# Kernel tuning notes

Measured on AMD Instinct MI355X. Metric: run time of the kernel, lower is better.

Reference implementation:

```python
import jax, jax.numpy as jnp
import numpy as np

# Constants from the torch module __init__
FACE_INDS = np.array([[0, 1, 2, 3], [0, 4, 2, 6], [0, 1, 4, 5],
                      [1, 3, 5, 7], [2, 3, 6, 7], [4, 5, 6, 7]])  # (6,4)
N_GRID = 11
N_POINTS = N_GRID * N_GRID        # 121
N_FACE = 6
N_KP_HAND = 21
N_CONTACTS = 10
ITA = 0.2
IND1 = np.array([0, 1, 2, 3])
IND2 = np.array([1, 2, 3, 0])


def _bilinear_grid():
    # grid[p, k] = bilinear weights for the 4 face corners, p over 11x11 (u,v)
    g = []
    for u in np.linspace(0.0, 1.0, N_GRID):
        for v in np.linspace(0.0, 1.0, N_GRID):
            g.append([v * (1 - u), v * u, (1 - v) * (1 - u), u * (1 - v)])
    return jnp.asarray(np.array(g, dtype=np.float32))  # (121, 4)


def setup_inputs() -> dict:
    key = jax.random.key(0)
    poses = jax.random.normal(key, (8192, N_KP_HAND + 8, 3), dtype=jnp.float32)
    return {"poses": poses}


def affinity_loss(poses):
    bs = poses.shape[0]
    hand = poses[:, :N_KP_HAND, :]          # (bs, 21, 3)
    obj = poses[:, N_KP_HAND:, :]           # (bs, 8, 3)

    # --- sample_face_points: bilinear sample 121 pts on each of the 6 faces ---
    grid = _bilinear_grid().astype(poses.dtype)        # (121, 4)
    faces = obj[:, FACE_INDS, :]                        # (bs, 6, 4, 3)
    face_points = jnp.einsum('bfkc,pk->bfpc', faces, grid)  # (bs, 6, 121, 3)
    obj_pts = face_points.reshape(bs, N_FACE * N_POINTS, 3)  # (bs, 726, 3)

    xx = jnp.sum(hand * hand, axis=-1)                  # (bs, 21)
    yy = jnp.sum(obj_pts * obj_pts, axis=-1)            # (bs, 726)
    zz = jnp.einsum('bic,bjc->bij', hand, obj_pts)      # (bs, 21, 726)
    pdist = jnp.sqrt(xx[:, :, None] + yy[:, None, :] - 2.0 * zz + 1e-6)
    pdist = pdist.reshape(bs, N_KP_HAND, N_FACE, N_POINTS)

    # --- per (hand kp, face) nearest face point, then global top-10 contacts ---
    dist_h2f = jnp.min(pdist, axis=3)                   # (bs, 21, 6)
    idxs_h2f = jnp.argmin(pdist, axis=3)                # (bs, 21, 6)
    flat = dist_h2f.reshape(bs, N_KP_HAND * N_FACE)     # (bs, 126)
    order = jnp.argsort(flat, axis=1)[:, :N_CONTACTS]   # (bs, 10)
    dist = jnp.take_along_axis(flat, order, axis=1)     # (bs, 10)
    inds_hand = order // N_FACE
    inds_face = order % N_FACE
    b = jnp.arange(bs)[:, None]
    ind_obj = idxs_h2f[b, inds_hand, inds_face]                     # (bs, 10)
    obj_contacts = obj_pts[b, inds_face * N_POINTS + ind_obj]       # (bs, 10, 3)

    # --- get_obj_info: axis endpoints and mean edge length of the bbox ---
    points1 = obj[:, :4, :].mean(axis=1)                # (bs, 3)
    points2 = obj[:, 4:, :].mean(axis=1)                # (bs, 3)
    l1 = jnp.linalg.norm(obj[:, IND1] - obj[:, IND2], axis=-1).mean(1, keepdims=True)
    l2 = jnp.linalg.norm(obj[:, IND1 + 4] - obj[:, IND2 + 4], axis=-1).mean(1, keepdims=True)
    length = (l1 + l2) * 0.5                            # (bs, 1)

    mask1 = (dist < length * ITA).astype(poses.dtype)   # (bs, 10)
    mask = mask1[:, :, None] * mask1[:, None, :]        # (bs, 10, 10)

    direct_vec = points2 - points1                      # (bs, 3)
    dv_norm = jnp.linalg.norm(direct_vec, axis=1, keepdims=True)  # (bs, 1)
    normed_dv = direct_vec / (dv_norm + 1e-5)
    vec_contacts = obj_contacts - points1[:, None, :]   # (bs, 10, 3)
    inner = jnp.sum(direct_vec[:, None, :] * vec_contacts, axis=-1)  # (bs, 10)
    t = inner / (dv_norm + 1e-5)                        # (bs, 10)
    r = points1[:, None, :] + normed_dv[:, None, :] * t[:, :, None]  # (bs, 10, 3)
    normal_vec = obj_contacts - r
    normal_vec = normal_vec / (jnp.linalg.norm(normal_vec, axis=2, keepdims=True) + 1e-5)
    cos_sim = jnp.einsum('bic,bjc->bij', normal_vec, normal_vec)  # (bs, 10, 10)

    return (cos_sim * mask).sum() / (mask.sum() + 1.0)


def reference(poses):
    return affinity_loss(poses)
```

## Files before the change

### kernel.cpp

```cpp
#include <hip/hip_runtime.h>
#include <math.h>

#define NGRID   11
#define NPAIR   126
#define NCONT   10

#define NSUB    64
#define NBUK    128
#define WS_SUB  16
#define WS_BUK  128
#define WS_WORDS (WS_BUK + 2 * NBUK)

#define NBUCKET 256

typedef float v2f __attribute__((ext_vector_type(2)));
#define FMA2(a,b,c) __builtin_elementwise_fma((a),(b),(c))
#define MAX2(a,b)   __builtin_elementwise_max((a),(b))
#define SP2(x)      ((v2f){(x),(x)})

__device__ __forceinline__ int last_hit(unsigned old, unsigned quota) {
    const unsigned r = old + 1u - quota;
    return (r == 0u) || (r == 0xAAAAAAAAu);
}

__device__ __constant__ int4 c_face4[6] = {
    {0,1,2,3},{0,4,2,6},{0,1,4,5},{1,3,5,7},{2,3,6,7},{4,5,6,7}};
__device__ __constant__ float c_U[NGRID] = {
    0.0f,0.1f,0.2f,0.3f,0.4f,0.5f,0.6f,0.7f,0.8f,0.9f,1.0f};

__global__ void zero_ws_kernel(float* ws, int n) {
    int t = blockIdx.x * 256 + threadIdx.x;
    if (t < n) ws[t] = 0.0f;
}

__device__ __forceinline__ void coefs_from_face(
        const float4* __restrict__ Ff, float hx, float hy, float hz,
        float& C00, float& C10, float& C01, float& C11,
        float& C20, float& C02, float& C21, float& C12, float& C22) {
    const float4 F0 = Ff[0], F1 = Ff[1], F2 = Ff[2],
                 F3 = Ff[3], F4 = Ff[4], F5 = Ff[5];
    const float hx2 = 2.0f * hx, hy2 = 2.0f * hy, hz2 = 2.0f * hz;
    const float ha2 = fmaf(hx2, F0.x, fmaf(hy2, F0.y, hz2 * F0.z));
    const float hb2 = fmaf(hx2, F1.x, fmaf(hy2, F1.y, hz2 * F1.z));
    const float hc2 = fmaf(hx2, F2.x, fmaf(hy2, F2.y, hz2 * F2.z));
    const float hd2 = fmaf(hx2, F3.x, fmaf(hy2, F3.y, hz2 * F3.z));
    C00 = ha2 - F0.w;
    C10 = hb2 - F4.x;
    C01 = hc2 - F4.y;
    C11 = hd2 - F4.z;
    C20 = -F1.w;  C02 = -F2.w;  C21 = -F4.w;  C12 = -F5.x;  C22 = -F3.w;
}

__launch_bounds__(256)
__global__ void affinity_kernel(const float* __restrict__ poses,
                                float* __restrict__ ws,
                                float* __restrict__ out,
                                int bs, int mode) {
    const int t    = threadIdx.x;
    const int half = t >> 7;
    const int t0   = t & 127;
    const int batch = blockIdx.x * 2 + half;
    const bool valid = batch < bs;

    __shared__ float    sh_pose[2][88];
    __shared__ float4   sh_face[2][36];
    __shared__ float    sh_thr[2][2];
    __shared__ int      sh_ru[2][128];
    __shared__ int      sh_cpair[2][128];
    __shared__ unsigned sh_cnt[2], sh_cnt2[2];
    __shared__ unsigned sh_key[2][128];
    __shared__ float    sh_cont[2][128][3];
    __shared__ float    sh_win[2][NCONT][3];
    __shared__ float    sh_nd[2][2];
    __shared__ int      sh_last;
    __shared__ double   sh_rn[4], sh_rd[4];

    if (valid && t0 < 87) sh_pose[half][t0] = poses[(size_t)batch * 87 + t0];
    if (t0 == 127) { sh_cnt[half] = 0u; sh_cnt2[half] = 0u; }
    __syncthreads();

    const float* hand = sh_pose[half];
    const float* obj  = sh_pose[half] + 63;

    if (valid && t0 < 6) {
        const int4 F = c_face4[t0];
        float C0[3], C1[3], C2[3], C3[3];
        #pragma unroll
        for (int c = 0; c < 3; ++c) {
            C0[c] = obj[F.x * 3 + c];
            C1[c] = obj[F.y * 3 + c];
            C2[c] = obj[F.z * 3 + c];
            C3[c] = obj[F.w * 3 + c];
        }
        float av[3], bv[3], cv[3], dv[3];
        #pragma unroll
        for (int c = 0; c < 3; ++c) {
            av[c] = C2[c];
            bv[c] = C3[c] - C2[c];
            cv[c] = C0[c] - C2[c];
            dv[c] = C1[c] - C0[c] - C3[c] + C2[c];
        }
        float aa=0.f,bb=0.f,cc=0.f,dd=0.f,ab=0.f,ac=0.f,ad=0.f,bc=0.f,bd=0.f,cd=0.f;
        #pragma unroll
        for (int c = 0; c < 3; ++c) {
            aa += av[c]*av[c]; bb += bv[c]*bv[c];
            cc += cv[c]*cv[c]; dd += dv[c]*dv[c];
            ab += av[c]*bv[c]; ac += av[c]*cv[c];
            ad += av[c]*dv[c]; bc += bv[c]*cv[c];
            bd += bv[c]*dv[c]; cd += cv[c]*dv[c];
        }
        float4* Ff = &sh_face[half][t0 * 6];
        Ff[0] = make_float4(av[0], av[1], av[2], aa);
        Ff[1] = make_float4(bv[0], bv[1], bv[2], bb);
        Ff[2] = make_float4(cv[0], cv[1], cv[2], cc);
        Ff[3] = make_float4(dv[0], dv[1], dv[2], dd);
        Ff[4] = make_float4(2.f*ab, 2.f*ac, 2.f*(ad+bc), 2.f*bd);
        Ff[5] = make_float4(2.f*cd, 0.f, 0.f, 0.f);
    }
    if (valid && t0 == 6) {
        float l1 = 0.0f, l2 = 0.0f;
        #pragma unroll
        for (int e = 0; e < 4; ++e) {
            const int a = e, b2 = (e + 1) & 3;
            {
                const float dx = obj[a*3+0]-obj[b2*3+0];
                const float dy = obj[a*3+1]-obj[b2*3+1];
                const float dz = obj[a*3+2]-obj[b2*3+2];
                l1 += sqrtf(dx*dx + dy*dy + dz*dz);
            }
            {
                const float dx = obj[(a+4)*3+0]-obj[(b2+4)*3+0];
                const float dy = obj[(a+4)*3+1]-obj[(b2+4)*3+1];
                const float dz = obj[(a+4)*3+2]-obj[(b2+4)*3+2];
                l2 += sqrtf(dx*dx + dy*dy + dz*dz);
            }
        }
        l1 *= 0.25f; l2 *= 0.25f;
        const float L02 = (l1 + l2) * 0.5f * 0.2f;
        sh_thr[half][0] = L02 * L02 - 1e-6f + 1e-2f;
        sh_thr[half][1] = L02;
    }
    __syncthreads();

    if (valid && t0 < NPAIR) {
        const int i = t0 / 6;
        const int f = t0 - i * 6;
        const float hx = hand[i*3+0], hy = hand[i*3+1], hz = hand[i*3+2];
        const float xx = hx*hx + hy*hy + hz*hz;
        float C00,C10,C01,C11,C20,C02,C21,C12,C22;
        coefs_from_face(&sh_face[half][f*6], hx, hy, hz,
                        C00,C10,C01,C11,C20,C02,C21,C12,C22);

        const float U[NGRID] = {0.0f,0.1f,0.2f,0.3f,0.4f,0.5f,
                                0.6f,0.7f,0.8f,0.9f,1.0f};
        float qb = -3.0e38f;
        int   ru = 0;
        #pragma unroll
        for (int rp = 0; rp < 5; ++rp) {
            const v2f u2 = (v2f){U[2*rp], U[2*rp+1]};
            const v2f A2 = FMA2(FMA2(SP2(C22), u2, SP2(C12)), u2, SP2(C02));
            const v2f A1 = FMA2(FMA2(SP2(C21), u2, SP2(C11)), u2, SP2(C01));
            const v2f A0 = FMA2(FMA2(SP2(C20), u2, SP2(C10)), u2, SP2(C00));
            v2f m2 = A0;
            #pragma unroll
            for (int iv = 1; iv < NGRID; ++iv) {
                const v2f vv = SP2(U[iv]);
                m2 = MAX2(m2, FMA2(FMA2(A2, vv, A1), vv, A0));
            }
            if (m2.x > qb) { qb = m2.x; ru = 2*rp; }
            if (m2.y > qb) { qb = m2.y; ru = 2*rp + 1; }
        }
        {
            const float u = 1.0f;
            const float A2 = fmaf(fmaf(C22,u,C12),u,C02);
            const float A1 = fmaf(fmaf(C21,u,C11),u,C01);
            const float A0 = fmaf(fmaf(C20,u,C10),u,C00);
            float m1 = A0;
            #pragma unroll
            for (int iv = 1; iv < NGRID; ++iv)
                m1 = fmaxf(m1, fmaf(fmaf(A2,U[iv],A1),U[iv],A0));
            if (m1 > qb) { qb = m1; ru = 10; }
        }
        sh_ru[half][t0] = ru;
        const float d2s = xx - qb;
        if (d2s < sh_thr[half][0]) {
            const unsigned s = atomicAdd(&sh_cnt[half], 1u);
            sh_cpair[half][s] = t0;
        }
    }
    __syncthreads();

    {
        const int cnt = (int)sh_cnt[half];
        if (t0 < cnt) {
            const int pair = sh_cpair[half][t0];
            const int i  = pair / 6;
            const int f  = pair - 6 * i;
            const int ru = sh_ru[half][pair];
            const float hx = hand[i*3+0], hy = hand[i*3+1], hz = hand[i*3+2];
            float C00,C10,C01,C11,C20,C02,C21,C12,C22;
            coefs_from_face(&sh_face[half][f*6], hx, hy, hz,
                            C00,C10,C01,C11,C20,C02,C21,C12,C22);
            const float u  = c_U[ru];
            const float A2 = fmaf(fmaf(C22,u,C12),u,C02);
            const float A1 = fmaf(fmaf(C21,u,C11),u,C01);
            const float A0 = fmaf(fmaf(C20,u,C10),u,C00);
            const float U[NGRID] = {0.0f,0.1f,0.2f,0.3f,0.4f,0.5f,
                                    0.6f,0.7f,0.8f,0.9f,1.0f};
            float qr = A0; int vb = 0;
            #pragma unroll
            for (int iv = 1; iv < NGRID; ++iv) {
                const float q = fmaf(fmaf(A2,U[iv],A1),U[iv],A0);
                if (q > qr) { qr = q; vb = iv; }
            }
            const double du = ru * 0.1;
            const double dv = vb * 0.1;
            const float w0 = (float)(dv * (1.0 - du));
            const float w1 = (float)(dv * du);
            const float w2 = (float)((1.0 - dv) * (1.0 - du));
            const float w3 = (float)(du * (1.0 - dv));
            const int4 F = c_face4[f];
            const int i0 = F.x*3, i1 = F.y*3, i2 = F.z*3, i3 = F.w*3;
            const float cx = w0*obj[i0+0]+w1*obj[i1+0]+w2*obj[i2+0]+w3*obj[i3+0];
            const float cy = w0*obj[i0+1]+w1*obj[i1+1]+w2*obj[i2+1]+w3*obj[i3+1];
            const float cz = w0*obj[i0+2]+w1*obj[i1+2]+w2*obj[i2+2]+w3*obj[i3+2];
            const float xx = hx*hx + hy*hy + hz*hz;
            const float yy = cx*cx + cy*cy + cz*cz;
            const float zz = hx*cx + hy*cy + hz*cz;
            const float d2e = (xx + yy) - 2.0f * zz;
            const float dist = sqrtf(d2e + 1e-6f);
            if (dist < sh_thr[half][1]) {
                const unsigned s2 = atomicAdd(&sh_cnt2[half], 1u);
                const float d2k = fmaxf(d2e, 0.0f);
                sh_key[half][s2] = (__float_as_uint(d2k) & 0xFFFFFF80u)
                                 | (unsigned)pair;
                sh_cont[half][s2][0] = cx;
                sh_cont[half][s2][1] = cy;
                sh_cont[half][s2][2] = cz;
            }
        }
    }
    __syncthreads();

    const int n2 = (int)sh_cnt2[half];
    if (t0 < n2) {
        const unsigned ke = sh_key[half][t0];
        int rank = 0;
        for (int j = 0; j < n2; ++j) rank += (sh_key[half][j] < ke) ? 1 : 0;
        if (rank < NCONT) {
            sh_win[half][rank][0] = sh_cont[half][t0][0];
            sh_win[half][rank][1] = sh_cont[half][t0][1];
            sh_win[half][rank][2] = sh_cont[half][t0][2];
        }
    }
    __syncthreads();

    const int kwin = n2 < NCONT ? n2 : NCONT;
    float px = 0.f, py = 0.f, pz = 0.f;
    if (valid && t0 < kwin) {
        const float cx = sh_win[half][t0][0];
        const float cy = sh_win[half][t0][1];
        const float cz = sh_win[half][t0][2];
        const float p1x = (((obj[0] +obj[3]) +obj[6]) +obj[9]) *0.25f;
        const float p1y = (((obj[1] +obj[4]) +obj[7]) +obj[10])*0.25f;
        const float p1z = (((obj[2] +obj[5]) +obj[8]) +obj[11])*0.25f;
        const float p2x = (((obj[12]+obj[15])+obj[18])+obj[21])*0.25f;
        const float p2y = (((obj[13]+obj[16])+obj[19])+obj[22])*0.25f;
        const float p2z = (((obj[14]+obj[17])+obj[20])+obj[23])*0.25f;
        const float dvx = p2x-p1x, dvy = p2y-p1y, dvz = p2z-p1z;
        const float dvn = sqrtf(dvx*dvx + dvy*dvy + dvz*dvz);
        const float den = dvn + 1e-5f;
        const float ndx = dvx/den, ndy = dvy/den, ndz = dvz/den;
        const float vcx = cx-p1x, vcy = cy-p1y, vcz = cz-p1z;
        const float inner = dvx*vcx + dvy*vcy + dvz*vcz;
        const float tp = inner / den;
        const float rx = p1x + ndx*tp, ry = p1y + ndy*tp, rz = p1z + ndz*tp;
        float nvx = cx-rx, nvy = cy-ry, nvz = cz-rz;
        const float nvn = sqrtf(nvx*nvx + nvy*nvy + nvz*nvz) + 1e-5f;
        px = nvx / nvn; py = nvy / nvn; pz = nvz / nvn;
    }
    if (t0 < 64) {
        #pragma unroll
        for (int off = 32; off >= 1; off >>= 1) {
            px += __shfl_xor(px, off, 64);
            py += __shfl_xor(py, off, 64);
            pz += __shfl_xor(pz, off, 64);
        }
        if (t0 == 0) {
            sh_nd[half][0] = px*px + py*py + pz*pz;
            sh_nd[half][1] = (float)(kwin * kwin);
        }
    }
    __syncthreads();

    if (t == 0) {
        sh_last = 0;
        const float num = sh_nd[0][0] + sh_nd[1][0];
        const float dnm = sh_nd[0][1] + sh_nd[1][1];
        const int b = blockIdx.x;
        if (mode) {
            float* bkt = ws + WS_BUK + 2 * (b & (NBUK - 1));
            const float r0 = atomicAdd(bkt + 0, num);
            const float r1 = atomicAdd(bkt + 1, dnm);
            asm volatile("" :: "v"(r0), "v"(r1) : "memory");
            unsigned* subs = (unsigned*)ws + WS_SUB;
            const unsigned nb = gridDim.x;
            const unsigned g  = (unsigned)b & (NSUB - 1);
            const unsigned quota = (nb - 1u - g) / NSUB + 1u;
            const unsigned old = atomicAdd(subs + g, 1u);
            if (last_hit(old, quota)) {
                const unsigned ngroups = nb < NSUB ? nb : NSUB;
                const unsigned m2 = atomicAdd((unsigned*)ws, 1u);
                if (last_hit(m2, ngroups)) sh_last = 1;
            }
        } else {
            float* bucket = ws + 2 * (b & (NBUCKET - 1));
            atomicAdd(bucket + 0, num);
            atomicAdd(bucket + 1, dnm);
        }
    }
    __syncthreads();

    if (sh_last) {
        double n = 0.0, d = 0.0;
        if (t < NBUK) {
            float* bkt = ws + WS_BUK + 2 * t;
            n = (double)atomicAdd(bkt + 0, 0.0f);
            d = (double)atomicAdd(bkt + 1, 0.0f);
        }
        #pragma unroll
        for (int off = 32; off >= 1; off >>= 1) {
            n += __shfl_xor(n, off, 64);
            d += __shfl_xor(d, off, 64);
        }
        const int w = t >> 6;
        if ((t & 63) == 0) { sh_rn[w] = n; sh_rd[w] = d; }
        __syncthreads();
        if (t == 0) {
            const double nn = sh_rn[0] + sh_rn[1] + sh_rn[2] + sh_rn[3];
            const double dd = sh_rd[0] + sh_rd[1] + sh_rd[2] + sh_rd[3];
            out[0] = (float)(nn / (dd + 1.0));
        }
    }
}

__launch_bounds__(1024)
__global__ void finalize_kernel(const float* __restrict__ ws,
                                float* __restrict__ out, int nslot) {
    const int t = threadIdx.x;
    __shared__ double sh_n[16], sh_d[16];
    double n = 0.0, d = 0.0;
    for (int k = t; k < nslot; k += 1024) {
        n += (double)ws[2 * k + 0];
        d += (double)ws[2 * k + 1];
    }
    #pragma unroll
    for (int off = 32; off >= 1; off >>= 1) {
        n += __shfl_xor(n, off, 64);
        d += __shfl_xor(d, off, 64);
    }
    const int w = t >> 6;
    if ((t & 63) == 0) { sh_n[w] = n; sh_d[w] = d; }
    __syncthreads();
    if (t == 0) {
        double nn = 0.0, dd = 0.0;
        #pragma unroll
        for (int i = 0; i < 16; ++i) { nn += sh_n[i]; dd += sh_d[i]; }
        out[0] = (float)(nn / (dd + 1.0));
    }
}

extern "C" void kernel_launch(void* const* d_in, const int* in_sizes, int n_in,
                              void* d_out, int out_size, void* d_ws, size_t ws_size,
                              hipStream_t stream) {
    const float* poses = (const float*)d_in[0];
    float* out = (float*)d_out;
    float* ws  = (float*)d_ws;
    const int bs = in_sizes[0] / 87;
    const int nblk = (bs + 1) / 2;

    if (ws_size >= (size_t)WS_WORDS * sizeof(float)) {
        hipLaunchKernelGGL(affinity_kernel, dim3(nblk), dim3(256), 0, stream,
                           poses, ws, out, bs, 1);
    } else {
        hipLaunchKernelGGL(zero_ws_kernel, dim3(1), dim3(256), 0, stream,
                           ws, NBUCKET * 2);
        hipLaunchKernelGGL(affinity_kernel, dim3(nblk), dim3(256), 0, stream,
                           poses, ws, out, bs, 0);
        hipLaunchKernelGGL(finalize_kernel, dim3(1), dim3(1024), 0, stream,
                           ws, out, NBUCKET);
    }
}
```

Before: 76.69 us.

## Process one batch per 128-thread block and finish reduction in one wave

Switches from two batch elements per 256-thread block to one batch element per 128-thread block, doubling the grid to bs blocks. The upper wave exits early after the top-k selection, and the final contribution and last-block reduction use wave shuffles instead of shared memory plus block barriers. The aim is to cut the per-block barrier and shared-memory traffic and give the scheduler smaller blocks, at the cost of twice as many blocks and twice as many global atomic arrivals on the completion counters.

```diff
diff --git a/kernel.cpp b/kernel.cpp
--- a/kernel.cpp
+++ b/kernel.cpp
@@ -51,39 +51,33 @@
     C20 = -F1.w;  C02 = -F2.w;  C21 = -F4.w;  C12 = -F5.x;  C22 = -F3.w;
 }
 
-__launch_bounds__(256)
+__launch_bounds__(128)
 __global__ void affinity_kernel(const float* __restrict__ poses,
                                 float* __restrict__ ws,
                                 float* __restrict__ out,
                                 int bs, int mode) {
-    const int t    = threadIdx.x;
-    const int half = t >> 7;
-    const int t0   = t & 127;
-    const int batch = blockIdx.x * 2 + half;
-    const bool valid = batch < bs;
-
-    __shared__ float    sh_pose[2][88];
-    __shared__ float4   sh_face[2][36];
-    __shared__ float    sh_thr[2][2];
-    __shared__ int      sh_ru[2][128];
-    __shared__ int      sh_cpair[2][128];
-    __shared__ unsigned sh_cnt[2], sh_cnt2[2];
-    __shared__ unsigned sh_key[2][128];
-    __shared__ float    sh_cont[2][128][3];
-    __shared__ float    sh_win[2][NCONT][3];
-    __shared__ float    sh_nd[2][2];
-    __shared__ int      sh_last;
-    __shared__ double   sh_rn[4], sh_rd[4];
-
-    if (valid && t0 < 87) sh_pose[half][t0] = poses[(size_t)batch * 87 + t0];
-    if (t0 == 127) { sh_cnt[half] = 0u; sh_cnt2[half] = 0u; }
-    __syncthreads();
-
-    const float* hand = sh_pose[half];
-    const float* obj  = sh_pose[half] + 63;
-
-    if (valid && t0 < 6) {
-        const int4 F = c_face4[t0];
+    const int t = threadIdx.x;
+    const int b = blockIdx.x;
+
+    __shared__ float    sh_pose[88];
+    __shared__ float4   sh_face[36];
+    __shared__ float    sh_thr[2];
+    __shared__ int      sh_ru[128];
+    __shared__ int      sh_cpair[128];
+    __shared__ unsigned sh_cnt, sh_cnt2;
+    __shared__ unsigned sh_key[128];
+    __shared__ float    sh_cont[128][3];
+    __shared__ float    sh_win[NCONT][3];
+
+    if (t < 87) sh_pose[t] = poses[(size_t)b * 87 + t];
+    if (t == 127) { sh_cnt = 0u; sh_cnt2 = 0u; }
+    __syncthreads();
+
+    const float* hand = sh_pose;
+    const float* obj  = sh_pose + 63;
+
+    if (t < 6) {
+        const int4 F = c_face4[t];
         float C0[3], C1[3], C2[3], C3[3];
         #pragma unroll
         for (int c = 0; c < 3; ++c) {
@@ -109,7 +103,7 @@
             ad += av[c]*dv[c]; bc += bv[c]*cv[c];
             bd += bv[c]*dv[c]; cd += cv[c]*dv[c];
         }
-        float4* Ff = &sh_face[half][t0 * 6];
+        float4* Ff = &sh_face[t * 6];
         Ff[0] = make_float4(av[0], av[1], av[2], aa);
         Ff[1] = make_float4(bv[0], bv[1], bv[2], bb);
         Ff[2] = make_float4(cv[0], cv[1], cv[2], cc);
@@ -117,7 +111,7 @@
         Ff[4] = make_float4(2.f*ab, 2.f*ac, 2.f*(ad+bc), 2.f*bd);
         Ff[5] = make_float4(2.f*cd, 0.f, 0.f, 0.f);
     }
-    if (valid && t0 == 6) {
+    if (t == 6) {
         float l1 = 0.0f, l2 = 0.0f;
         #pragma unroll
         for (int e = 0; e < 4; ++e) {
@@ -137,18 +131,18 @@
         }
         l1 *= 0.25f; l2 *= 0.25f;
         const float L02 = (l1 + l2) * 0.5f * 0.2f;
-        sh_thr[half][0] = L02 * L02 - 1e-6f + 1e-2f;
-        sh_thr[half][1] = L02;
-    }
-    __syncthreads();
-
-    if (valid && t0 < NPAIR) {
-        const int i = t0 / 6;
-        const int f = t0 - i * 6;
+        sh_thr[0] = L02 * L02 - 1e-6f + 1e-2f;
+        sh_thr[1] = L02;
+    }
+    __syncthreads();
+
+    if (t < NPAIR) {
+        const int i = t / 6;
+        const int f = t - i * 6;
         const float hx = hand[i*3+0], hy = hand[i*3+1], hz = hand[i*3+2];
         const float xx = hx*hx + hy*hy + hz*hz;
         float C00,C10,C01,C11,C20,C02,C21,C12,C22;
-        coefs_from_face(&sh_face[half][f*6], hx, hy, hz,
+        coefs_from_face(&sh_face[f*6], hx, hy, hz,
                         C00,C10,C01,C11,C20,C02,C21,C12,C22);
 
         const float U[NGRID] = {0.0f,0.1f,0.2f,0.3f,0.4f,0.5f,
@@ -181,25 +175,25 @@
                 m1 = fmaxf(m1, fmaf(fmaf(A2,U[iv],A1),U[iv],A0));
             if (m1 > qb) { qb = m1; ru = 10; }
         }
-        sh_ru[half][t0] = ru;
+        sh_ru[t] = ru;
         const float d2s = xx - qb;
-        if (d2s < sh_thr[half][0]) {
-            const unsigned s = atomicAdd(&sh_cnt[half], 1u);
-            sh_cpair[half][s] = t0;
+        if (d2s < sh_thr[0]) {
+            const unsigned s = atomicAdd(&sh_cnt, 1u);
+            sh_cpair[s] = t;
         }
     }
     __syncthreads();
 
     {
-        const int cnt = (int)sh_cnt[half];
-        if (t0 < cnt) {
-            const int pair = sh_cpair[half][t0];
+        const int cnt = (int)sh_cnt;
+        if (t < cnt) {
+            const int pair = sh_cpair[t];
             const int i  = pair / 6;
             const int f  = pair - 6 * i;
-            const int ru = sh_ru[half][pair];
+            const int ru = sh_ru[pair];
             const float hx = hand[i*3+0], hy = hand[i*3+1], hz = hand[i*3+2];
             float C00,C10,C01,C11,C20,C02,C21,C12,C22;
-            coefs_from_face(&sh_face[half][f*6], hx, hy, hz,
+            coefs_from_face(&sh_face[f*6], hx, hy, hz,
                             C00,C10,C01,C11,C20,C02,C21,C12,C22);
             const float u  = c_U[ru];
             const float A2 = fmaf(fmaf(C22,u,C12),u,C02);
@@ -229,38 +223,40 @@
             const float zz = hx*cx + hy*cy + hz*cz;
             const float d2e = (xx + yy) - 2.0f * zz;
             const float dist = sqrtf(d2e + 1e-6f);
-            if (dist < sh_thr[half][1]) {
-                const unsigned s2 = atomicAdd(&sh_cnt2[half], 1u);
+            if (dist < sh_thr[1]) {
+                const unsigned s2 = atomicAdd(&sh_cnt2, 1u);
                 const float d2k = fmaxf(d2e, 0.0f);
-                sh_key[half][s2] = (__float_as_uint(d2k) & 0xFFFFFF80u)
-                                 | (unsigned)pair;
-                sh_cont[half][s2][0] = cx;
-                sh_cont[half][s2][1] = cy;
-                sh_cont[half][s2][2] = cz;
-            }
-        }
-    }
-    __syncthreads();
-
-    const int n2 = (int)sh_cnt2[half];
-    if (t0 < n2) {
-        const unsigned ke = sh_key[half][t0];
+                sh_key[s2] = (__float_as_uint(d2k) & 0xFFFFFF80u)
+                           | (unsigned)pair;
+                sh_cont[s2][0] = cx;
+                sh_cont[s2][1] = cy;
+                sh_cont[s2][2] = cz;
+            }
+        }
+    }
+    __syncthreads();
+
+    const int n2 = (int)sh_cnt2;
+    if (t < n2) {
+        const unsigned ke = sh_key[t];
         int rank = 0;
-        for (int j = 0; j < n2; ++j) rank += (sh_key[half][j] < ke) ? 1 : 0;
+        for (int j = 0; j < n2; ++j) rank += (sh_key[j] < ke) ? 1 : 0;
         if (rank < NCONT) {
-            sh_win[half][rank][0] = sh_cont[half][t0][0];
-            sh_win[half][rank][1] = sh_cont[half][t0][1];
-            sh_win[half][rank][2] = sh_cont[half][t0][2];
-        }
-    }
-    __syncthreads();
+            sh_win[rank][0] = sh_cont[t][0];
+            sh_win[rank][1] = sh_cont[t][1];
+            sh_win[rank][2] = sh_cont[t][2];
+        }
+    }
+    __syncthreads();
+
+    if (t >= 64) return;
 
     const int kwin = n2 < NCONT ? n2 : NCONT;
     float px = 0.f, py = 0.f, pz = 0.f;
-    if (valid && t0 < kwin) {
-        const float cx = sh_win[half][t0][0];
-        const float cy = sh_win[half][t0][1];
-        const float cz = sh_win[half][t0][2];
+    if (t < kwin) {
+        const float cx = sh_win[t][0];
+        const float cy = sh_win[t][1];
+        const float cz = sh_win[t][2];
         const float p1x = (((obj[0] +obj[3]) +obj[6]) +obj[9]) *0.25f;
         const float p1y = (((obj[1] +obj[4]) +obj[7]) +obj[10])*0.25f;
         const float p1z = (((obj[2] +obj[5]) +obj[8]) +obj[11])*0.25f;
@@ -279,25 +275,17 @@
         const float nvn = sqrtf(nvx*nvx + nvy*nvy + nvz*nvz) + 1e-5f;
         px = nvx / nvn; py = nvy / nvn; pz = nvz / nvn;
     }
-    if (t0 < 64) {
-        #pragma unroll
-        for (int off = 32; off >= 1; off >>= 1) {
-            px += __shfl_xor(px, off, 64);
-            py += __shfl_xor(py, off, 64);
-            pz += __shfl_xor(pz, off, 64);
-        }
-        if (t0 == 0) {
-            sh_nd[half][0] = px*px + py*py + pz*pz;
-            sh_nd[half][1] = (float)(kwin * kwin);
-        }
-    }
-    __syncthreads();
-
+    #pragma unroll
+    for (int off = 32; off >= 1; off >>= 1) {
+        px += __shfl_xor(px, off, 64);
+        py += __shfl_xor(py, off, 64);
+        pz += __shfl_xor(pz, off, 64);
+    }
+
+    int last = 0;
     if (t == 0) {
-        sh_last = 0;
-        const float num = sh_nd[0][0] + sh_nd[1][0];
-        const float dnm = sh_nd[0][1] + sh_nd[1][1];
-        const int b = blockIdx.x;
+        const float num = px*px + py*py + pz*pz;
+        const float dnm = (float)(kwin * kwin);
         if (mode) {
             float* bkt = ws + WS_BUK + 2 * (b & (NBUK - 1));
             const float r0 = atomicAdd(bkt + 0, num);
@@ -311,7 +299,7 @@
             if (last_hit(old, quota)) {
                 const unsigned ngroups = nb < NSUB ? nb : NSUB;
                 const unsigned m2 = atomicAdd((unsigned*)ws, 1u);
-                if (last_hit(m2, ngroups)) sh_last = 1;
+                if (last_hit(m2, ngroups)) last = 1;
             }
         } else {
             float* bucket = ws + 2 * (b & (NBUCKET - 1));
@@ -319,28 +307,22 @@
             atomicAdd(bucket + 1, dnm);
         }
     }
-    __syncthreads();
-
-    if (sh_last) {
+    last = __shfl(last, 0, 64);
+
+    if (last) {
         double n = 0.0, d = 0.0;
-        if (t < NBUK) {
-            float* bkt = ws + WS_BUK + 2 * t;
-            n = (double)atomicAdd(bkt + 0, 0.0f);
-            d = (double)atomicAdd(bkt + 1, 0.0f);
+        #pragma unroll
+        for (int c = 0; c < 2; ++c) {
+            float* bkt = ws + WS_BUK + 2 * (c * 64 + t);
+            n += (double)atomicAdd(bkt + 0, 0.0f);
+            d += (double)atomicAdd(bkt + 1, 0.0f);
         }
         #pragma unroll
         for (int off = 32; off >= 1; off >>= 1) {
             n += __shfl_xor(n, off, 64);
             d += __shfl_xor(d, off, 64);
         }
-        const int w = t >> 6;
-        if ((t & 63) == 0) { sh_rn[w] = n; sh_rd[w] = d; }
-        __syncthreads();
-        if (t == 0) {
-            const double nn = sh_rn[0] + sh_rn[1] + sh_rn[2] + sh_rn[3];
-            const double dd = sh_rd[0] + sh_rd[1] + sh_rd[2] + sh_rd[3];
-            out[0] = (float)(nn / (dd + 1.0));
-        }
+        if (t == 0) out[0] = (float)(n / (d + 1.0));
     }
 }
 
@@ -377,15 +359,14 @@
     float* out = (float*)d_out;
     float* ws  = (float*)d_ws;
     const int bs = in_sizes[0] / 87;
-    const int nblk = (bs + 1) / 2;
 
     if (ws_size >= (size_t)WS_WORDS * sizeof(float)) {
-        hipLaunchKernelGGL(affinity_kernel, dim3(nblk), dim3(256), 0, stream,
+        hipLaunchKernelGGL(affinity_kernel, dim3(bs), dim3(128), 0, stream,
                            poses, ws, out, bs, 1);
     } else {
         hipLaunchKernelGGL(zero_ws_kernel, dim3(1), dim3(256), 0, stream,
                            ws, NBUCKET * 2);
-        hipLaunchKernelGGL(affinity_kernel, dim3(nblk), dim3(256), 0, stream,
+        hipLaunchKernelGGL(affinity_kernel, dim3(bs), dim3(128), 0, stream,
                            poses, ws, out, bs, 0);
         hipLaunchKernelGGL(finalize_kernel, dim3(1), dim3(1024), 0, stream,
                            ws, out, NBUCKET);
```

Result: slower. 88.81 us (+15.8%).

## Remove face-precompute barrier and fuse ranking with normal computation

Applied to the files above, without the earlier changes.

Each pair thread now recomputes its face coefficients and the length threshold from the shared pose, which removes the per-face shared-memory precompute stage and one block barrier. The candidate's u-index is packed into the candidate record instead of a separate shared array. Top-10 ranking is merged with the normal-vector accumulation inside one wavefront, removing another barrier and the winner buffer. The final cross-block reduction runs on a single wave using shuffles instead of shared memory and barriers. The cost is redundant ALU work per thread and more register pressure.

```diff
diff --git a/kernel.cpp b/kernel.cpp
--- a/kernel.cpp
+++ b/kernel.cpp
@@ -33,22 +33,101 @@
     if (t < n) ws[t] = 0.0f;
 }
 
-__device__ __forceinline__ void coefs_from_face(
-        const float4* __restrict__ Ff, float hx, float hy, float hz,
+__device__ __forceinline__ void pair_coefs(
+        const float* __restrict__ obj, float hx, float hy, float hz, int f,
         float& C00, float& C10, float& C01, float& C11,
         float& C20, float& C02, float& C21, float& C12, float& C22) {
-    const float4 F0 = Ff[0], F1 = Ff[1], F2 = Ff[2],
-                 F3 = Ff[3], F4 = Ff[4], F5 = Ff[5];
-    const float hx2 = 2.0f * hx, hy2 = 2.0f * hy, hz2 = 2.0f * hz;
-    const float ha2 = fmaf(hx2, F0.x, fmaf(hy2, F0.y, hz2 * F0.z));
-    const float hb2 = fmaf(hx2, F1.x, fmaf(hy2, F1.y, hz2 * F1.z));
-    const float hc2 = fmaf(hx2, F2.x, fmaf(hy2, F2.y, hz2 * F2.z));
-    const float hd2 = fmaf(hx2, F3.x, fmaf(hy2, F3.y, hz2 * F3.z));
-    C00 = ha2 - F0.w;
-    C10 = hb2 - F4.x;
-    C01 = hc2 - F4.y;
-    C11 = hd2 - F4.z;
-    C20 = -F1.w;  C02 = -F2.w;  C21 = -F4.w;  C12 = -F5.x;  C22 = -F3.w;
+    const int4 F = c_face4[f];
+    float av[3], bv[3], cv[3], dv[3];
+    #pragma unroll
+    for (int c = 0; c < 3; ++c) {
+        const float P0 = obj[F.x * 3 + c];
+        const float P1 = obj[F.y * 3 + c];
+        const float P2 = obj[F.z * 3 + c];
+        const float P3 = obj[F.w * 3 + c];
+        av[c] = P2;
+        bv[c] = P3 - P2;
+        cv[c] = P0 - P2;
+        dv[c] = P1 - P0 - P3 + P2;
+    }
+    float aa=0.f,bb=0.f,cc=0.f,dd=0.f,ab=0.f,ac=0.f,ad=0.f,bc=0.f,bd=0.f,cd=0.f;
+    #pragma unroll
+    for (int c = 0; c < 3; ++c) {
+        aa += av[c]*av[c]; bb += bv[c]*bv[c];
+        cc += cv[c]*cv[c]; dd += dv[c]*dv[c];
+        ab += av[c]*bv[c]; ac += av[c]*cv[c];
+        ad += av[c]*dv[c]; bc += bv[c]*cv[c];
+        bd += bv[c]*dv[c]; cd += cv[c]*dv[c];
+    }
+    const float hx2 = 2.0f*hx, hy2 = 2.0f*hy, hz2 = 2.0f*hz;
+    const float ha2 = fmaf(hx2, av[0], fmaf(hy2, av[1], hz2*av[2]));
+    const float hb2 = fmaf(hx2, bv[0], fmaf(hy2, bv[1], hz2*bv[2]));
+    const float hc2 = fmaf(hx2, cv[0], fmaf(hy2, cv[1], hz2*cv[2]));
+    const float hd2 = fmaf(hx2, dv[0], fmaf(hy2, dv[1], hz2*dv[2]));
+    C00 = ha2 - aa;
+    C10 = hb2 - 2.f*ab;
+    C01 = hc2 - 2.f*ac;
+    C11 = hd2 - 2.f*(ad + bc);
+    C20 = -bb;  C02 = -cc;  C21 = -2.f*bd;  C12 = -2.f*cd;  C22 = -dd;
+}
+
+__device__ __forceinline__ float length_thr(const float* __restrict__ obj) {
+    float l1 = 0.0f, l2 = 0.0f;
+    #pragma unroll
+    for (int e = 0; e < 4; ++e) {
+        const int a = e, b2 = (e + 1) & 3;
+        {
+            const float dx = obj[a*3+0]-obj[b2*3+0];
+            const float dy = obj[a*3+1]-obj[b2*3+1];
+            const float dz = obj[a*3+2]-obj[b2*3+2];
+            l1 += sqrtf(dx*dx + dy*dy + dz*dz);
+        }
+        {
+            const float dx = obj[(a+4)*3+0]-obj[(b2+4)*3+0];
+            const float dy = obj[(a+4)*3+1]-obj[(b2+4)*3+1];
+            const float dz = obj[(a+4)*3+2]-obj[(b2+4)*3+2];
+            l2 += sqrtf(dx*dx + dy*dy + dz*dz);
+        }
+    }
+    l1 *= 0.25f; l2 *= 0.25f;
+    return (l1 + l2) * 0.5f * 0.2f;
+}
+
+__device__ __forceinline__ void exact_contact(
+        const float* __restrict__ obj, const float* __restrict__ hand,
+        int pair, int ru, float& cx, float& cy, float& cz, float& d2e) {
+    const int i = pair / 6;
+    const int f = pair - 6 * i;
+    const float hx = hand[i*3+0], hy = hand[i*3+1], hz = hand[i*3+2];
+    float C00,C10,C01,C11,C20,C02,C21,C12,C22;
+    pair_coefs(obj, hx, hy, hz, f, C00,C10,C01,C11,C20,C02,C21,C12,C22);
+    const float u  = c_U[ru];
+    const float A2 = fmaf(fmaf(C22,u,C12),u,C02);
+    const float A1 = fmaf(fmaf(C21,u,C11),u,C01);
+    const float A0 = fmaf(fmaf(C20,u,C10),u,C00);
+    const float U[NGRID] = {0.0f,0.1f,0.2f,0.3f,0.4f,0.5f,
+                            0.6f,0.7f,0.8f,0.9f,1.0f};
+    float qr = A0; int vb = 0;
+    #pragma unroll
+    for (int iv = 1; iv < NGRID; ++iv) {
+        const float q = fmaf(fmaf(A2,U[iv],A1),U[iv],A0);
+        if (q > qr) { qr = q; vb = iv; }
+    }
+    const double du = ru * 0.1;
+    const double dv = vb * 0.1;
+    const float w0 = (float)(dv * (1.0 - du));
+    const float w1 = (float)(dv * du);
+    const float w2 = (float)((1.0 - dv) * (1.0 - du));
+    const float w3 = (float)(du * (1.0 - dv));
+    const int4 F = c_face4[f];
+    const int i0 = F.x*3, i1 = F.y*3, i2 = F.z*3, i3 = F.w*3;
+    cx = w0*obj[i0+0]+w1*obj[i1+0]+w2*obj[i2+0]+w3*obj[i3+0];
+    cy = w0*obj[i0+1]+w1*obj[i1+1]+w2*obj[i2+1]+w3*obj[i3+1];
+    cz = w0*obj[i0+2]+w1*obj[i1+2]+w2*obj[i2+2]+w3*obj[i3+2];
+    const float xx = hx*hx + hy*hy + hz*hz;
+    const float yy = cx*cx + cy*cy + cz*cz;
+    const float zz = hx*cx + hy*cy + hz*cz;
+    d2e = (xx + yy) - 2.0f * zz;
 }
 
 __launch_bounds__(256)
@@ -63,17 +142,11 @@
     const bool valid = batch < bs;
 
     __shared__ float    sh_pose[2][88];
-    __shared__ float4   sh_face[2][36];
-    __shared__ float    sh_thr[2][2];
-    __shared__ int      sh_ru[2][128];
-    __shared__ int      sh_cpair[2][128];
+    __shared__ unsigned sh_cand[2][128];
     __shared__ unsigned sh_cnt[2], sh_cnt2[2];
     __shared__ unsigned sh_key[2][128];
     __shared__ float    sh_cont[2][128][3];
-    __shared__ float    sh_win[2][NCONT][3];
     __shared__ float    sh_nd[2][2];
-    __shared__ int      sh_last;
-    __shared__ double   sh_rn[4], sh_rd[4];
 
     if (valid && t0 < 87) sh_pose[half][t0] = poses[(size_t)batch * 87 + t0];
     if (t0 == 127) { sh_cnt[half] = 0u; sh_cnt2[half] = 0u; }
@@ -82,74 +155,17 @@
     const float* hand = sh_pose[half];
     const float* obj  = sh_pose[half] + 63;
 
-    if (valid && t0 < 6) {
-        const int4 F = c_face4[t0];
-        float C0[3], C1[3], C2[3], C3[3];
-        #pragma unroll
-        for (int c = 0; c < 3; ++c) {
-            C0[c] = obj[F.x * 3 + c];
-            C1[c] = obj[F.y * 3 + c];
-            C2[c] = obj[F.z * 3 + c];
-            C3[c] = obj[F.w * 3 + c];
-        }
-        float av[3], bv[3], cv[3], dv[3];
-        #pragma unroll
-        for (int c = 0; c < 3; ++c) {
-            av[c] = C2[c];
-            bv[c] = C3[c] - C2[c];
-            cv[c] = C0[c] - C2[c];
-            dv[c] = C1[c] - C0[c] - C3[c] + C2[c];
-        }
-        float aa=0.f,bb=0.f,cc=0.f,dd=0.f,ab=0.f,ac=0.f,ad=0.f,bc=0.f,bd=0.f,cd=0.f;
-        #pragma unroll
-        for (int c = 0; c < 3; ++c) {
-            aa += av[c]*av[c]; bb += bv[c]*bv[c];
-            cc += cv[c]*cv[c]; dd += dv[c]*dv[c];
-            ab += av[c]*bv[c]; ac += av[c]*cv[c];
-            ad += av[c]*dv[c]; bc += bv[c]*cv[c];
-            bd += bv[c]*dv[c]; cd += cv[c]*dv[c];
-        }
-        float4* Ff = &sh_face[half][t0 * 6];
-        Ff[0] = make_float4(av[0], av[1], av[2], aa);
-        Ff[1] = make_float4(bv[0], bv[1], bv[2], bb);
-        Ff[2] = make_float4(cv[0], cv[1], cv[2], cc);
-        Ff[3] = make_float4(dv[0], dv[1], dv[2], dd);
-        Ff[4] = make_float4(2.f*ab, 2.f*ac, 2.f*(ad+bc), 2.f*bd);
-        Ff[5] = make_float4(2.f*cd, 0.f, 0.f, 0.f);
-    }
-    if (valid && t0 == 6) {
-        float l1 = 0.0f, l2 = 0.0f;
-        #pragma unroll
-        for (int e = 0; e < 4; ++e) {
-            const int a = e, b2 = (e + 1) & 3;
-            {
-                const float dx = obj[a*3+0]-obj[b2*3+0];
-                const float dy = obj[a*3+1]-obj[b2*3+1];
-                const float dz = obj[a*3+2]-obj[b2*3+2];
-                l1 += sqrtf(dx*dx + dy*dy + dz*dz);
-            }
-            {
-                const float dx = obj[(a+4)*3+0]-obj[(b2+4)*3+0];
-                const float dy = obj[(a+4)*3+1]-obj[(b2+4)*3+1];
-                const float dz = obj[(a+4)*3+2]-obj[(b2+4)*3+2];
-                l2 += sqrtf(dx*dx + dy*dy + dz*dz);
-            }
-        }
-        l1 *= 0.25f; l2 *= 0.25f;
-        const float L02 = (l1 + l2) * 0.5f * 0.2f;
-        sh_thr[half][0] = L02 * L02 - 1e-6f + 1e-2f;
-        sh_thr[half][1] = L02;
-    }
-    __syncthreads();
-
+    float L02 = 0.f;
     if (valid && t0 < NPAIR) {
+        L02 = length_thr(obj);
+        const float thrF = L02 * L02 - 1e-6f + 1e-2f;
+
         const int i = t0 / 6;
         const int f = t0 - i * 6;
         const float hx = hand[i*3+0], hy = hand[i*3+1], hz = hand[i*3+2];
         const float xx = hx*hx + hy*hy + hz*hz;
         float C00,C10,C01,C11,C20,C02,C21,C12,C22;
-        coefs_from_face(&sh_face[half][f*6], hx, hy, hz,
-                        C00,C10,C01,C11,C20,C02,C21,C12,C22);
+        pair_coefs(obj, hx, hy, hz, f, C00,C10,C01,C11,C20,C02,C21,C12,C22);
 
         const float U[NGRID] = {0.0f,0.1f,0.2f,0.3f,0.4f,0.5f,
                                 0.6f,0.7f,0.8f,0.9f,1.0f};
@@ -171,21 +187,19 @@
             if (m2.y > qb) { qb = m2.y; ru = 2*rp + 1; }
         }
         {
-            const float u = 1.0f;
-            const float A2 = fmaf(fmaf(C22,u,C12),u,C02);
-            const float A1 = fmaf(fmaf(C21,u,C11),u,C01);
-            const float A0 = fmaf(fmaf(C20,u,C10),u,C00);
+            const float A2 = fmaf(fmaf(C22,1.f,C12),1.f,C02);
+            const float A1 = fmaf(fmaf(C21,1.f,C11),1.f,C01);
+            const float A0 = fmaf(fmaf(C20,1.f,C10),1.f,C00);
             float m1 = A0;
             #pragma unroll
             for (int iv = 1; iv < NGRID; ++iv)
                 m1 = fmaxf(m1, fmaf(fmaf(A2,U[iv],A1),U[iv],A0));
             if (m1 > qb) { qb = m1; ru = 10; }
         }
-        sh_ru[half][t0] = ru;
         const float d2s = xx - qb;
-        if (d2s < sh_thr[half][0]) {
+        if (d2s < thrF) {
             const unsigned s = atomicAdd(&sh_cnt[half], 1u);
-            sh_cpair[half][s] = t0;
+            sh_cand[half][s] = (unsigned)t0 | ((unsigned)ru << 8);
         }
     }
     __syncthreads();
@@ -193,47 +207,16 @@
     {
         const int cnt = (int)sh_cnt[half];
         if (t0 < cnt) {
-            const int pair = sh_cpair[half][t0];
-            const int i  = pair / 6;
-            const int f  = pair - 6 * i;
-            const int ru = sh_ru[half][pair];
-            const float hx = hand[i*3+0], hy = hand[i*3+1], hz = hand[i*3+2];
-            float C00,C10,C01,C11,C20,C02,C21,C12,C22;
-            coefs_from_face(&sh_face[half][f*6], hx, hy, hz,
-                            C00,C10,C01,C11,C20,C02,C21,C12,C22);
-            const float u  = c_U[ru];
-            const float A2 = fmaf(fmaf(C22,u,C12),u,C02);
-            const float A1 = fmaf(fmaf(C21,u,C11),u,C01);
-            const float A0 = fmaf(fmaf(C20,u,C10),u,C00);
-            const float U[NGRID] = {0.0f,0.1f,0.2f,0.3f,0.4f,0.5f,
-                                    0.6f,0.7f,0.8f,0.9f,1.0f};
-            float qr = A0; int vb = 0;
-            #pragma unroll
-            for (int iv = 1; iv < NGRID; ++iv) {
-                const float q = fmaf(fmaf(A2,U[iv],A1),U[iv],A0);
-                if (q > qr) { qr = q; vb = iv; }
-            }
-            const double du = ru * 0.1;
-            const double dv = vb * 0.1;
-            const float w0 = (float)(dv * (1.0 - du));
-            const float w1 = (float)(dv * du);
-            const float w2 = (float)((1.0 - dv) * (1.0 - du));
-            const float w3 = (float)(du * (1.0 - dv));
-            const int4 F = c_face4[f];
-            const int i0 = F.x*3, i1 = F.y*3, i2 = F.z*3, i3 = F.w*3;
-            const float cx = w0*obj[i0+0]+w1*obj[i1+0]+w2*obj[i2+0]+w3*obj[i3+0];
-            const float cy = w0*obj[i0+1]+w1*obj[i1+1]+w2*obj[i2+1]+w3*obj[i3+1];
-            const float cz = w0*obj[i0+2]+w1*obj[i1+2]+w2*obj[i2+2]+w3*obj[i3+2];
-            const float xx = hx*hx + hy*hy + hz*hz;
-            const float yy = cx*cx + cy*cy + cz*cz;
-            const float zz = hx*cx + hy*cy + hz*cz;
-            const float d2e = (xx + yy) - 2.0f * zz;
+            const unsigned rec = sh_cand[half][t0];
+            const int pair = rec & 0xFF;
+            const int ru   = rec >> 8;
+            float cx, cy, cz, d2e;
+            exact_contact(obj, hand, pair, ru, cx, cy, cz, d2e);
             const float dist = sqrtf(d2e + 1e-6f);
-            if (dist < sh_thr[half][1]) {
+            if (dist < L02) {
                 const unsigned s2 = atomicAdd(&sh_cnt2[half], 1u);
-                const float d2k = fmaxf(d2e, 0.0f);
-                sh_key[half][s2] = (__float_as_uint(d2k) & 0xFFFFFF80u)
-                                 | (unsigned)pair;
+                sh_key[half][s2] = (__float_as_uint(fmaxf(d2e, 0.0f))
+                                    & 0xFFFFFF80u) | (unsigned)pair;
                 sh_cont[half][s2][0] = cx;
                 sh_cont[half][s2][1] = cy;
                 sh_cont[half][s2][2] = cz;
@@ -242,49 +225,52 @@
     }
     __syncthreads();
 
-    const int n2 = (int)sh_cnt2[half];
-    if (t0 < n2) {
-        const unsigned ke = sh_key[half][t0];
-        int rank = 0;
-        for (int j = 0; j < n2; ++j) rank += (sh_key[half][j] < ke) ? 1 : 0;
-        if (rank < NCONT) {
-            sh_win[half][rank][0] = sh_cont[half][t0][0];
-            sh_win[half][rank][1] = sh_cont[half][t0][1];
-            sh_win[half][rank][2] = sh_cont[half][t0][2];
-        }
-    }
-    __syncthreads();
-
-    const int kwin = n2 < NCONT ? n2 : NCONT;
-    float px = 0.f, py = 0.f, pz = 0.f;
-    if (valid && t0 < kwin) {
-        const float cx = sh_win[half][t0][0];
-        const float cy = sh_win[half][t0][1];
-        const float cz = sh_win[half][t0][2];
-        const float p1x = (((obj[0] +obj[3]) +obj[6]) +obj[9]) *0.25f;
-        const float p1y = (((obj[1] +obj[4]) +obj[7]) +obj[10])*0.25f;
-        const float p1z = (((obj[2] +obj[5]) +obj[8]) +obj[11])*0.25f;
-        const float p2x = (((obj[12]+obj[15])+obj[18])+obj[21])*0.25f;
-        const float p2y = (((obj[13]+obj[16])+obj[19])+obj[22])*0.25f;
-        const float p2z = (((obj[14]+obj[17])+obj[20])+obj[23])*0.25f;
-        const float dvx = p2x-p1x, dvy = p2y-p1y, dvz = p2z-p1z;
-        const float dvn = sqrtf(dvx*dvx + dvy*dvy + dvz*dvz);
-        const float den = dvn + 1e-5f;
-        const float ndx = dvx/den, ndy = dvy/den, ndz = dvz/den;
-        const float vcx = cx-p1x, vcy = cy-p1y, vcz = cz-p1z;
-        const float inner = dvx*vcx + dvy*vcy + dvz*vcz;
-        const float tp = inner / den;
-        const float rx = p1x + ndx*tp, ry = p1y + ndy*tp, rz = p1z + ndz*tp;
-        float nvx = cx-rx, nvy = cy-ry, nvz = cz-rz;
-        const float nvn = sqrtf(nvx*nvx + nvy*nvy + nvz*nvz) + 1e-5f;
-        px = nvx / nvn; py = nvy / nvn; pz = nvz / nvn;
-    }
     if (t0 < 64) {
-        #pragma unroll
-        for (int off = 32; off >= 1; off >>= 1) {
-            px += __shfl_xor(px, off, 64);
-            py += __shfl_xor(py, off, 64);
-            pz += __shfl_xor(pz, off, 64);
+        const int n2   = (int)sh_cnt2[half];
+        const int kwin = n2 < NCONT ? n2 : NCONT;
+        float px = 0.f, py = 0.f, pz = 0.f;
+        if (valid && n2 > 0) {
+            const float p1x = (((obj[0] +obj[3]) +obj[6]) +obj[9]) *0.25f;
+            const float p1y = (((obj[1] +obj[4]) +obj[7]) +obj[10])*0.25f;
+            const float p1z = (((obj[2] +obj[5]) +obj[8]) +obj[11])*0.25f;
+            const float p2x = (((obj[12]+obj[15])+obj[18])+obj[21])*0.25f;
+            const float p2y = (((obj[13]+obj[16])+obj[19])+obj[22])*0.25f;
+            const float p2z = (((obj[14]+obj[17])+obj[20])+obj[23])*0.25f;
+            const float dvx = p2x-p1x, dvy = p2y-p1y, dvz = p2z-p1z;
+            const float dvn = sqrtf(dvx*dvx + dvy*dvy + dvz*dvz);
+            const float den = dvn + 1e-5f;
+            const float ndx = dvx/den, ndy = dvy/den, ndz = dvz/den;
+            #pragma unroll
+            for (int c = 0; c < 2; ++c) {
+                if (c == 1 && n2 <= 64) break;
+                const int idx = c * 64 + t0;
+                if (idx < n2) {
+                    const unsigned ke = sh_key[half][idx];
+                    int rank = 0;
+                    for (int j = 0; j < n2; ++j)
+                        rank += (sh_key[half][j] < ke) ? 1 : 0;
+                    if (rank < NCONT) {
+                        const float cx = sh_cont[half][idx][0];
+                        const float cy = sh_cont[half][idx][1];
+                        const float cz = sh_cont[half][idx][2];
+                        const float vcx = cx-p1x, vcy = cy-p1y, vcz = cz-p1z;
+                        const float inner = dvx*vcx + dvy*vcy + dvz*vcz;
+                        const float tp = inner / den;
+                        const float rx = p1x + ndx*tp, ry = p1y + ndy*tp,
+                                    rz = p1z + ndz*tp;
+                        const float nvx = cx-rx, nvy = cy-ry, nvz = cz-rz;
+                        const float nvn = sqrtf(nvx*nvx + nvy*nvy + nvz*nvz)
+                                        + 1e-5f;
+                        px += nvx / nvn; py += nvy / nvn; pz += nvz / nvn;
+                    }
+                }
+            }
+            #pragma unroll
+            for (int off = 32; off >= 1; off >>= 1) {
+                px += __shfl_xor(px, off, 64);
+                py += __shfl_xor(py, off, 64);
+                pz += __shfl_xor(pz, off, 64);
+            }
         }
         if (t0 == 0) {
             sh_nd[half][0] = px*px + py*py + pz*pz;
@@ -293,8 +279,10 @@
     }
     __syncthreads();
 
+    if (t >= 64) return;
+
+    int last = 0;
     if (t == 0) {
-        sh_last = 0;
         const float num = sh_nd[0][0] + sh_nd[1][0];
         const float dnm = sh_nd[0][1] + sh_nd[1][1];
         const int b = blockIdx.x;
@@ -311,7 +299,7 @@
             if (last_hit(old, quota)) {
                 const unsigned ngroups = nb < NSUB ? nb : NSUB;
                 const unsigned m2 = atomicAdd((unsigned*)ws, 1u);
-                if (last_hit(m2, ngroups)) sh_last = 1;
+                if (last_hit(m2, ngroups)) last = 1;
             }
         } else {
             float* bucket = ws + 2 * (b & (NBUCKET - 1));
@@ -319,28 +307,22 @@
             atomicAdd(bucket + 1, dnm);
         }
     }
-    __syncthreads();
-
-    if (sh_last) {
+    last = __shfl(last, 0, 64);
+
+    if (last) {
         double n = 0.0, d = 0.0;
-        if (t < NBUK) {
-            float* bkt = ws + WS_BUK + 2 * t;
-            n = (double)atomicAdd(bkt + 0, 0.0f);
-            d = (double)atomicAdd(bkt + 1, 0.0f);
+        #pragma unroll
+        for (int c = 0; c < 2; ++c) {
+            float* bkt = ws + WS_BUK + 2 * (c * 64 + t);
+            n += (double)atomicAdd(bkt + 0, 0.0f);
+            d += (double)atomicAdd(bkt + 1, 0.0f);
         }
         #pragma unroll
         for (int off = 32; off >= 1; off >>= 1) {
             n += __shfl_xor(n, off, 64);
             d += __shfl_xor(d, off, 64);
         }
-        const int w = t >> 6;
-        if ((t & 63) == 0) { sh_rn[w] = n; sh_rd[w] = d; }
-        __syncthreads();
-        if (t == 0) {
-            const double nn = sh_rn[0] + sh_rn[1] + sh_rn[2] + sh_rn[3];
-            const double dd = sh_rd[0] + sh_rd[1] + sh_rd[2] + sh_rd[3];
-            out[0] = (float)(nn / (dd + 1.0));
-        }
+        if (t == 0) out[0] = (float)(n / (d + 1.0));
     }
 }
 
```

Result: no change. 78.17 us (+1.9%).
